# Kernel optimization log

Hardware: AMD Instinct MI355X
Metric: run time of the kernel (lower is better)

Reference implementation:

```python
import jax, jax.numpy as jnp
import numpy as np

B, N, IN_DIM, HID = 16, 2048, 128, 128
EPS = 1e-5


def _layer(x, W, b, g, beta):
    # x: (B, N, d_in) -> (B, N, HID)
    h = jnp.einsum('bnd,dh->bnh', x, W) + b
    mu = jnp.mean(h, axis=-1, keepdims=True)
    var = jnp.mean((h - mu) ** 2, axis=-1, keepdims=True)
    h = (h - mu) * jax.lax.rsqrt(var + EPS) * g + beta
    return jax.nn.relu(h)


def setup_inputs() -> dict:
    key = jax.random.key(0)
    ks = jax.random.split(key, 8)
    x = jax.random.normal(ks[0], (B, N, IN_DIM), dtype=jnp.float32)
    adj = jax.random.uniform(ks[1], (B, N, N), dtype=jnp.float32)
    inp = {'x': x, 'adj': adj}
    dims = [IN_DIM, HID, HID]
    for i in range(3):
        d_in = dims[i]
        scale = 1.0 / np.sqrt(d_in)
        inp[f'W{i}'] = jax.random.uniform(ks[2 + i], (d_in, HID), dtype=jnp.float32, minval=-scale, maxval=scale)
        inp[f'b{i}'] = jax.random.uniform(ks[5 + i], (HID,), dtype=jnp.float32, minval=-scale, maxval=scale)
        inp[f'g{i}'] = jnp.ones((HID,), dtype=jnp.float32)
        inp[f'be{i}'] = jnp.zeros((HID,), dtype=jnp.float32)
    return inp


def reference(x, adj, W0, b0, g0, be0, W1, b1, g1, be1, W2, b2, g2, be2):
    params = [(W0, b0, g0, be0), (W1, b1, g1, be1), (W2, b2, g2, be2)]
    h = x
    for (W, b, g, beta) in params:
        h_agg = jnp.einsum('bnm,bmd->bnd', adj, h)  # dense adjacency aggregation
        h = _layer(h_agg, W, b, g, beta)
    return h
```

## Files before the change

kernel.cpp:

```cpp
#include <hip/hip_runtime.h>
#include <hip/hip_bf16.h>

typedef __bf16 bf16;
typedef __bf16 bf16x4 __attribute__((ext_vector_type(4)));
typedef __bf16 bf16x8 __attribute__((ext_vector_type(8)));
typedef float  f32x2  __attribute__((ext_vector_type(2)));
typedef float  f32x4  __attribute__((ext_vector_type(4)));

static constexpr int NB  = 16;
static constexpr int NN  = 2048;
static constexpr int HID = 128;

__device__ __forceinline__ void gload_lds16(const bf16* g, bf16* l) {
    __builtin_amdgcn_global_load_lds(
        (const __attribute__((address_space(1))) unsigned int*)g,
        (__attribute__((address_space(3))) unsigned int*)l, 16, 0, 0);
}

__global__ __launch_bounds__(256) void prep_wt(const float* __restrict__ W0,
                                               const float* __restrict__ W1,
                                               const float* __restrict__ W2,
                                               bf16* __restrict__ WT) {
    int l = blockIdx.x;
    const float* W = (l == 0) ? W0 : (l == 1) ? W1 : W2;
    bf16* out = WT + l * 128 * 128;
    int tid = threadIdx.x;
#pragma unroll
    for (int i = 0; i < 64; ++i) {
        int idx = i * 256 + tid;
        int k = idx >> 7, n = idx & 127;
        out[n * 128 + k] = (bf16)W[idx];
    }
}

template<typename TA>
__global__ __launch_bounds__(256) void small_gemm(const TA* __restrict__ A,
                                                  const bf16* __restrict__ WT,
                                                  bf16* __restrict__ tmpT) {
    __shared__ bf16 smem[2 * 128 * 72];
    bf16* As = smem;
    bf16* Bs = smem + 128 * 72;

    const int tid  = threadIdx.x;
    const int wave = tid >> 6, lane = tid & 63;
    const int c0 = lane & 15, q = lane >> 4;
    const int blk = blockIdx.x;
    const int row_g0 = blk * 128;

    f32x4 acc[2][8] = {};

    for (int kk = 0; kk < 2; ++kk) {
        const int k0 = kk * 64;
        if constexpr (sizeof(TA) == 4) {
#pragma unroll
            for (int i = 0; i < 8; ++i) {
                int flat = i * 1024 + tid * 4;
                int row = flat >> 6, col = flat & 63;
                f32x4 v = *(const f32x4*)(A + (size_t)(row_g0 + row) * 128 + k0 + col);
                bf16x4 o = { (bf16)v.x, (bf16)v.y, (bf16)v.z, (bf16)v.w };
                *(bf16x4*)(As + row * 72 + col) = o;
            }
        } else {
#pragma unroll
            for (int i = 0; i < 4; ++i) {
                int flat = i * 2048 + tid * 8;
                int row = flat >> 6, col = flat & 63;
                bf16x8 v = *(const bf16x8*)((const bf16*)A + (size_t)(row_g0 + row) * 128 + k0 + col);
                *(bf16x8*)(As + row * 72 + col) = v;
            }
        }
#pragma unroll
        for (int i = 0; i < 4; ++i) {
            int flat = i * 2048 + tid * 8;
            int row = flat >> 6, col = flat & 63;
            bf16x8 v = *(const bf16x8*)(WT + (size_t)row * 128 + k0 + col);
            *(bf16x8*)(Bs + row * 72 + col) = v;
        }
        __syncthreads();
#pragma unroll
        for (int ks = 0; ks < 2; ++ks) {
            bf16x8 af[2];
#pragma unroll
            for (int mt = 0; mt < 2; ++mt)
                af[mt] = *(const bf16x8*)(As + (wave * 32 + mt * 16 + c0) * 72 + ks * 32 + q * 8);
#pragma unroll
            for (int nt = 0; nt < 8; ++nt) {
                bf16x8 bfr = *(const bf16x8*)(Bs + (nt * 16 + c0) * 72 + ks * 32 + q * 8);
#pragma unroll
                for (int mt = 0; mt < 2; ++mt)
                    acc[mt][nt] = __builtin_amdgcn_mfma_f32_16x16x32_bf16(af[mt], bfr, acc[mt][nt], 0, 0, 0);
            }
        }
        __syncthreads();
    }

    bf16* Cs = smem;
#pragma unroll
    for (int mt = 0; mt < 2; ++mt) {
        int mbase = wave * 32 + mt * 16 + q * 4;
#pragma unroll
        for (int nt = 0; nt < 8; ++nt) {
            int n = nt * 16 + c0;
#pragma unroll
            for (int r = 0; r < 4; ++r)
                Cs[n * 136 + mbase + r] = (bf16)acc[mt][nt][r];
        }
    }
    __syncthreads();
    const int b    = blk >> 4;
    const int row0 = (blk & 15) * 128;
    bf16* outp = tmpT + (size_t)b * 128 * 2048;
#pragma unroll
    for (int i = 0; i < 8; ++i) {
        int flat = i * 2048 + tid * 8;
        int n = flat >> 7, m = flat & 127;
        bf16x8 v = *(const bf16x8*)(Cs + n * 136 + m);
        *(bf16x8*)(outp + (size_t)n * 2048 + row0 + m) = v;
    }
}

template<int AMODE>
__global__ __launch_bounds__(256, 2) void big_gemm(const float* __restrict__ Af,
                                                   bf16* __restrict__ adjB,
                                                   const bf16* __restrict__ Bt,
                                                   float* __restrict__ part) {
    __shared__ bf16 As[128 * 64];
    __shared__ bf16 Bs[128 * 64];

    const int tid  = threadIdx.x;
    const int wave = tid >> 6, lane = tid & 63;
    const int c0 = lane & 15, q = lane >> 4;
    const int m0  = blockIdx.x * 128;
    const int ksp = blockIdx.y;
    const int b   = blockIdx.z;
    const size_t abase = (size_t)b * NN * NN;
    const bf16* Btb = Bt + (size_t)b * HID * NN;
    const int mrow = (wave >> 1) * 64, ncol = (wave & 1) * 64;

    f32x4 acc[4][4] = {};

    int prow[4], pcb[4];
#pragma unroll
    for (int j = 0; j < 4; ++j) {
        int p = j * 256 + wave * 64 + lane;
        prow[j] = p >> 3;
        pcb[j]  = (p & 7) ^ (prow[j] & 7);
    }
    const int ldsbase = wave * 64 * 8;

    for (int kk = 0; kk < 16; ++kk) {
        const int k0 = ksp * 1024 + kk * 64;
        if constexpr (AMODE == 1) {
#pragma unroll
            for (int j = 0; j < 4; ++j) {
                int g = j * 256 + tid;
                int grow = g >> 3, gcb = g & 7;
                const float* src = Af + abase + (size_t)(m0 + grow) * NN + k0 + gcb * 8;
                f32x4 a  = *(const f32x4*)src;
                f32x4 b2 = *(const f32x4*)(src + 4);
                bf16x8 o = {(bf16)a.x, (bf16)a.y, (bf16)a.z, (bf16)a.w,
                            (bf16)b2.x, (bf16)b2.y, (bf16)b2.z, (bf16)b2.w};
                *(bf16x8*)(As + (grow * 8 + (gcb ^ (grow & 7))) * 8) = o;
                *(bf16x8*)(adjB + abase + (size_t)(m0 + grow) * NN + k0 + gcb * 8) = o;
            }
        } else {
#pragma unroll
            for (int j = 0; j < 4; ++j)
                gload_lds16(adjB + abase + (size_t)(m0 + prow[j]) * NN + k0 + pcb[j] * 8,
                            As + j * 2048 + ldsbase);
        }
#pragma unroll
        for (int j = 0; j < 4; ++j)
            gload_lds16(Btb + (size_t)prow[j] * NN + k0 + pcb[j] * 8,
                        Bs + j * 2048 + ldsbase);
        __syncthreads();
#pragma unroll
        for (int ks = 0; ks < 2; ++ks) {
            bf16x8 af[4], bfr[4];
#pragma unroll
            for (int mt = 0; mt < 4; ++mt) {
                int row = mrow + mt * 16 + c0;
                int cb  = (ks * 4 + q) ^ (row & 7);
                af[mt] = *(const bf16x8*)(As + row * 64 + cb * 8);
            }
#pragma unroll
            for (int nt = 0; nt < 4; ++nt) {
                int row = ncol + nt * 16 + c0;
                int cb  = (ks * 4 + q) ^ (row & 7);
                bfr[nt] = *(const bf16x8*)(Bs + row * 64 + cb * 8);
            }
#pragma unroll
            for (int mt = 0; mt < 4; ++mt)
#pragma unroll
                for (int nt = 0; nt < 4; ++nt)
                    acc[mt][nt] = __builtin_amdgcn_mfma_f32_16x16x32_bf16(af[mt], bfr[nt], acc[mt][nt], 0, 0, 0);
        }
        __syncthreads();
    }

    float* pb = part + ((size_t)(ksp * NB + b) * NN + m0) * HID;
#pragma unroll
    for (int mt = 0; mt < 4; ++mt)
#pragma unroll
        for (int r = 0; r < 4; ++r) {
            int m = mrow + mt * 16 + q * 4 + r;
#pragma unroll
            for (int nt = 0; nt < 4; ++nt) {
                int n = ncol + nt * 16 + c0;
                pb[(size_t)m * HID + n] = acc[mt][nt][r];
            }
        }
}

template<bool OUTF32>
__global__ __launch_bounds__(256) void reduce_ln(const float* __restrict__ part,
                                                 const float* __restrict__ bias,
                                                 const float* __restrict__ gamma,
                                                 const float* __restrict__ betap,
                                                 bf16* __restrict__ outB,
                                                 float* __restrict__ outF) {
    const int tid = threadIdx.x, wave = tid >> 6, lane = tid & 63;
    const size_t row = (size_t)blockIdx.x * 4 + wave;
    const size_t off = row * HID + lane * 2;
    f32x2 p0 = *(const f32x2*)(part + off);
    f32x2 p1 = *(const f32x2*)(part + (size_t)NB * NN * HID + off);
    f32x2 bv = *(const f32x2*)(bias + lane * 2);
    float x0 = p0.x + p1.x + bv.x;
    float x1 = p0.y + p1.y + bv.y;
    float s1 = x0 + x1, s2 = x0 * x0 + x1 * x1;
#pragma unroll
    for (int o = 1; o < 64; o <<= 1) { s1 += __shfl_xor(s1, o); s2 += __shfl_xor(s2, o); }
    float mu  = s1 * (1.f / 128.f);
    float var = s2 * (1.f / 128.f) - mu * mu;
    float rs  = rsqrtf(var + 1e-5f);
    f32x2 gv = *(const f32x2*)(gamma + lane * 2);
    f32x2 be = *(const f32x2*)(betap + lane * 2);
    float o0 = fmaxf((x0 - mu) * rs * gv.x + be.x, 0.f);
    float o1 = fmaxf((x1 - mu) * rs * gv.y + be.y, 0.f);
    if constexpr (OUTF32) {
        f32x2 o = {o0, o1};
        *(f32x2*)(outF + off) = o;
    } else {
        bf16* p = outB + off;
        p[0] = (bf16)o0; p[1] = (bf16)o1;
    }
}

extern "C" void kernel_launch(void* const* d_in, const int* in_sizes, int n_in,
                              void* d_out, int out_size, void* d_ws, size_t ws_size,
                              hipStream_t stream) {
    const float* x   = (const float*)d_in[0];
    const float* adj = (const float*)d_in[1];
    const float* W[3]  = {(const float*)d_in[2],  (const float*)d_in[6],  (const float*)d_in[10]};
    const float* bb[3] = {(const float*)d_in[3],  (const float*)d_in[7],  (const float*)d_in[11]};
    const float* gg[3] = {(const float*)d_in[4],  (const float*)d_in[8],  (const float*)d_in[12]};
    const float* be[3] = {(const float*)d_in[5],  (const float*)d_in[9],  (const float*)d_in[13]};

    char* ws = (char*)d_ws;
    size_t off = 0;
    auto alloc = [&](size_t bytes) { char* p = ws + off; off = (off + bytes + 255) & ~(size_t)255; return p; };
    bf16*  WT   = (bf16*) alloc((size_t)3 * 128 * 128 * 2);
    bf16*  tmpT = (bf16*) alloc((size_t)NB * HID * NN * 2);
    bf16*  hB   = (bf16*) alloc((size_t)NB * NN * HID * 2);
    bf16*  adjB = (bf16*) alloc((size_t)NB * NN * NN * 2);
    float* part = (float*)alloc((size_t)2 * NB * NN * HID * 4);

    float* outF = (float*)d_out;

    prep_wt<<<3, 256, 0, stream>>>(W[0], W[1], W[2], WT);

    dim3 bg(16, 2, 16);
    small_gemm<float><<<256, 256, 0, stream>>>(x, WT, tmpT);
    big_gemm<1><<<bg, 256, 0, stream>>>(adj, adjB, tmpT, part);
    reduce_ln<false><<<8192, 256, 0, stream>>>(part, bb[0], gg[0], be[0], hB, nullptr);
    small_gemm<bf16><<<256, 256, 0, stream>>>(hB, WT + 128 * 128, tmpT);
    big_gemm<2><<<bg, 256, 0, stream>>>(adj, adjB, tmpT, part);
    reduce_ln<false><<<8192, 256, 0, stream>>>(part, bb[1], gg[1], be[1], hB, nullptr);
    small_gemm<bf16><<<256, 256, 0, stream>>>(hB, WT + 2 * 128 * 128, tmpT);
    big_gemm<2><<<bg, 256, 0, stream>>>(adj, adjB, tmpT, part);
    reduce_ln<true><<<8192, 256, 0, stream>>>(part, bb[2], gg[2], be[2], nullptr, outF);
}
```

Baseline: 583.9 us.

## Reorder to aggregate-then-project, fuse projection with LayerNorm, drop split-K

The per-layer order changes from (x·W then adj·) to (adj·h then ·W), which matches the reference order. The small projection GEMM is fused with bias, LayerNorm and ReLU into one kernel that writes the transposed bf16 activations for the next layer. The big adjacency GEMM drops the 2-way split-K and fp32 partial buffers in favour of 64-row tiles over the full K, writing bf16 output directly. This removes the separate reduce kernel and its fp32 partial traffic. The cost is a longer per-block K loop, smaller M tiles with less B reuse, and extra rounding from storing the aggregate in bf16.

New measurement: 556.6 us. 1.05x faster.

```diff
diff --git a/kernel.cpp b/kernel.cpp
--- a/kernel.cpp
+++ b/kernel.cpp
@@ -33,89 +33,26 @@
     }
 }
 
-template<typename TA>
-__global__ __launch_bounds__(256) void small_gemm(const TA* __restrict__ A,
-                                                  const bf16* __restrict__ WT,
-                                                  bf16* __restrict__ tmpT) {
-    __shared__ bf16 smem[2 * 128 * 72];
-    bf16* As = smem;
-    bf16* Bs = smem + 128 * 72;
-
-    const int tid  = threadIdx.x;
-    const int wave = tid >> 6, lane = tid & 63;
-    const int c0 = lane & 15, q = lane >> 4;
+__global__ __launch_bounds__(256) void prep_xt(const float* __restrict__ x,
+                                               bf16* __restrict__ xT) {
+    __shared__ bf16 T[128 * 136];
     const int blk = blockIdx.x;
-    const int row_g0 = blk * 128;
-
-    f32x4 acc[2][8] = {};
-
-    for (int kk = 0; kk < 2; ++kk) {
-        const int k0 = kk * 64;
-        if constexpr (sizeof(TA) == 4) {
-#pragma unroll
-            for (int i = 0; i < 8; ++i) {
-                int flat = i * 1024 + tid * 4;
-                int row = flat >> 6, col = flat & 63;
-                f32x4 v = *(const f32x4*)(A + (size_t)(row_g0 + row) * 128 + k0 + col);
-                bf16x4 o = { (bf16)v.x, (bf16)v.y, (bf16)v.z, (bf16)v.w };
-                *(bf16x4*)(As + row * 72 + col) = o;
-            }
-        } else {
-#pragma unroll
-            for (int i = 0; i < 4; ++i) {
-                int flat = i * 2048 + tid * 8;
-                int row = flat >> 6, col = flat & 63;
-                bf16x8 v = *(const bf16x8*)((const bf16*)A + (size_t)(row_g0 + row) * 128 + k0 + col);
-                *(bf16x8*)(As + row * 72 + col) = v;
-            }
-        }
-#pragma unroll
-        for (int i = 0; i < 4; ++i) {
-            int flat = i * 2048 + tid * 8;
-            int row = flat >> 6, col = flat & 63;
-            bf16x8 v = *(const bf16x8*)(WT + (size_t)row * 128 + k0 + col);
-            *(bf16x8*)(Bs + row * 72 + col) = v;
-        }
-        __syncthreads();
-#pragma unroll
-        for (int ks = 0; ks < 2; ++ks) {
-            bf16x8 af[2];
-#pragma unroll
-            for (int mt = 0; mt < 2; ++mt)
-                af[mt] = *(const bf16x8*)(As + (wave * 32 + mt * 16 + c0) * 72 + ks * 32 + q * 8);
-#pragma unroll
-            for (int nt = 0; nt < 8; ++nt) {
-                bf16x8 bfr = *(const bf16x8*)(Bs + (nt * 16 + c0) * 72 + ks * 32 + q * 8);
-#pragma unroll
-                for (int mt = 0; mt < 2; ++mt)
-                    acc[mt][nt] = __builtin_amdgcn_mfma_f32_16x16x32_bf16(af[mt], bfr, acc[mt][nt], 0, 0, 0);
-            }
-        }
-        __syncthreads();
-    }
-
-    bf16* Cs = smem;
-#pragma unroll
-    for (int mt = 0; mt < 2; ++mt) {
-        int mbase = wave * 32 + mt * 16 + q * 4;
-#pragma unroll
-        for (int nt = 0; nt < 8; ++nt) {
-            int n = nt * 16 + c0;
-#pragma unroll
-            for (int r = 0; r < 4; ++r)
-                Cs[n * 136 + mbase + r] = (bf16)acc[mt][nt][r];
-        }
+    const int b = blk >> 4, node0 = (blk & 15) * 128;
+    const int tid = threadIdx.x;
+    const float* xb = x + ((size_t)b * NN + node0) * HID;
+#pragma unroll
+    for (int i = 0; i < 64; ++i) {
+        int idx = i * 256 + tid;
+        int node = idx >> 7, hid = idx & 127;
+        T[hid * 136 + node] = (bf16)xb[(size_t)node * HID + hid];
     }
     __syncthreads();
-    const int b    = blk >> 4;
-    const int row0 = (blk & 15) * 128;
-    bf16* outp = tmpT + (size_t)b * 128 * 2048;
+    bf16* ob = xT + (size_t)b * HID * NN + node0;
 #pragma unroll
     for (int i = 0; i < 8; ++i) {
         int flat = i * 2048 + tid * 8;
-        int n = flat >> 7, m = flat & 127;
-        bf16x8 v = *(const bf16x8*)(Cs + n * 136 + m);
-        *(bf16x8*)(outp + (size_t)n * 2048 + row0 + m) = v;
+        int hid = flat >> 7, node = flat & 127;
+        *(bf16x8*)(ob + (size_t)hid * NN + node) = *(const bf16x8*)(T + hid * 136 + node);
     }
 }
 
@@ -123,21 +60,20 @@
 __global__ __launch_bounds__(256, 2) void big_gemm(const float* __restrict__ Af,
                                                    bf16* __restrict__ adjB,
                                                    const bf16* __restrict__ Bt,
-                                                   float* __restrict__ part) {
-    __shared__ bf16 As[128 * 64];
+                                                   bf16* __restrict__ g) {
+    __shared__ bf16 As[64 * 64];
     __shared__ bf16 Bs[128 * 64];
 
     const int tid  = threadIdx.x;
     const int wave = tid >> 6, lane = tid & 63;
     const int c0 = lane & 15, q = lane >> 4;
-    const int m0  = blockIdx.x * 128;
-    const int ksp = blockIdx.y;
-    const int b   = blockIdx.z;
+    const int m0 = blockIdx.x * 64;
+    const int b  = blockIdx.z;
     const size_t abase = (size_t)b * NN * NN;
     const bf16* Btb = Bt + (size_t)b * HID * NN;
-    const int mrow = (wave >> 1) * 64, ncol = (wave & 1) * 64;
-
-    f32x4 acc[4][4] = {};
+    const int wm = wave >> 1, wn = wave & 1;
+
+    f32x4 acc[2][4] = {};
 
     int prow[4], pcb[4];
 #pragma unroll
@@ -146,15 +82,15 @@
         prow[j] = p >> 3;
         pcb[j]  = (p & 7) ^ (prow[j] & 7);
     }
-    const int ldsbase = wave * 64 * 8;
-
-    for (int kk = 0; kk < 16; ++kk) {
-        const int k0 = ksp * 1024 + kk * 64;
+    const int ldsbase = wave * 512;
+
+    for (int kk = 0; kk < 32; ++kk) {
+        const int k0 = kk * 64;
         if constexpr (AMODE == 1) {
 #pragma unroll
-            for (int j = 0; j < 4; ++j) {
-                int g = j * 256 + tid;
-                int grow = g >> 3, gcb = g & 7;
+            for (int j = 0; j < 2; ++j) {
+                int gi = j * 256 + tid;
+                int grow = gi >> 3, gcb = gi & 7;
                 const float* src = Af + abase + (size_t)(m0 + grow) * NN + k0 + gcb * 8;
                 f32x4 a  = *(const f32x4*)src;
                 f32x4 b2 = *(const f32x4*)(src + 4);
@@ -165,7 +101,7 @@
             }
         } else {
 #pragma unroll
-            for (int j = 0; j < 4; ++j)
+            for (int j = 0; j < 2; ++j)
                 gload_lds16(adjB + abase + (size_t)(m0 + prow[j]) * NN + k0 + pcb[j] * 8,
                             As + j * 2048 + ldsbase);
         }
@@ -176,21 +112,21 @@
         __syncthreads();
 #pragma unroll
         for (int ks = 0; ks < 2; ++ks) {
-            bf16x8 af[4], bfr[4];
-#pragma unroll
-            for (int mt = 0; mt < 4; ++mt) {
-                int row = mrow + mt * 16 + c0;
+            bf16x8 af[2], bfr[4];
+#pragma unroll
+            for (int mt = 0; mt < 2; ++mt) {
+                int row = wm * 32 + mt * 16 + c0;
                 int cb  = (ks * 4 + q) ^ (row & 7);
                 af[mt] = *(const bf16x8*)(As + row * 64 + cb * 8);
             }
 #pragma unroll
             for (int nt = 0; nt < 4; ++nt) {
-                int row = ncol + nt * 16 + c0;
+                int row = wn * 64 + nt * 16 + c0;
                 int cb  = (ks * 4 + q) ^ (row & 7);
                 bfr[nt] = *(const bf16x8*)(Bs + row * 64 + cb * 8);
             }
 #pragma unroll
-            for (int mt = 0; mt < 4; ++mt)
+            for (int mt = 0; mt < 2; ++mt)
 #pragma unroll
                 for (int nt = 0; nt < 4; ++nt)
                     acc[mt][nt] = __builtin_amdgcn_mfma_f32_16x16x32_bf16(af[mt], bfr[nt], acc[mt][nt], 0, 0, 0);
@@ -198,51 +134,126 @@
         __syncthreads();
     }
 
-    float* pb = part + ((size_t)(ksp * NB + b) * NN + m0) * HID;
-#pragma unroll
-    for (int mt = 0; mt < 4; ++mt)
+    bf16* gb = g + ((size_t)b * NN + m0) * HID;
+#pragma unroll
+    for (int mt = 0; mt < 2; ++mt)
 #pragma unroll
         for (int r = 0; r < 4; ++r) {
-            int m = mrow + mt * 16 + q * 4 + r;
+            int m = wm * 32 + mt * 16 + q * 4 + r;
 #pragma unroll
             for (int nt = 0; nt < 4; ++nt) {
-                int n = ncol + nt * 16 + c0;
-                pb[(size_t)m * HID + n] = acc[mt][nt][r];
-            }
-        }
-}
-
-template<bool OUTF32>
-__global__ __launch_bounds__(256) void reduce_ln(const float* __restrict__ part,
-                                                 const float* __restrict__ bias,
-                                                 const float* __restrict__ gamma,
-                                                 const float* __restrict__ betap,
-                                                 bf16* __restrict__ outB,
-                                                 float* __restrict__ outF) {
-    const int tid = threadIdx.x, wave = tid >> 6, lane = tid & 63;
-    const size_t row = (size_t)blockIdx.x * 4 + wave;
-    const size_t off = row * HID + lane * 2;
-    f32x2 p0 = *(const f32x2*)(part + off);
-    f32x2 p1 = *(const f32x2*)(part + (size_t)NB * NN * HID + off);
-    f32x2 bv = *(const f32x2*)(bias + lane * 2);
-    float x0 = p0.x + p1.x + bv.x;
-    float x1 = p0.y + p1.y + bv.y;
-    float s1 = x0 + x1, s2 = x0 * x0 + x1 * x1;
-#pragma unroll
-    for (int o = 1; o < 64; o <<= 1) { s1 += __shfl_xor(s1, o); s2 += __shfl_xor(s2, o); }
-    float mu  = s1 * (1.f / 128.f);
-    float var = s2 * (1.f / 128.f) - mu * mu;
-    float rs  = rsqrtf(var + 1e-5f);
-    f32x2 gv = *(const f32x2*)(gamma + lane * 2);
-    f32x2 be = *(const f32x2*)(betap + lane * 2);
-    float o0 = fmaxf((x0 - mu) * rs * gv.x + be.x, 0.f);
-    float o1 = fmaxf((x1 - mu) * rs * gv.y + be.y, 0.f);
-    if constexpr (OUTF32) {
-        f32x2 o = {o0, o1};
-        *(f32x2*)(outF + off) = o;
-    } else {
-        bf16* p = outB + off;
-        p[0] = (bf16)o0; p[1] = (bf16)o1;
+                int n = wn * 64 + nt * 16 + c0;
+                gb[(size_t)m * HID + n] = (bf16)acc[mt][nt][r];
+            }
+        }
+}
+
+template<bool FINAL>
+__global__ __launch_bounds__(256) void small_ln(const bf16* __restrict__ gin,
+                                                const bf16* __restrict__ WT,
+                                                const float* __restrict__ bias,
+                                                const float* __restrict__ gamma,
+                                                const float* __restrict__ betap,
+                                                bf16* __restrict__ hT,
+                                                float* __restrict__ outF) {
+    __shared__ bf16 smem[2 * 128 * 72];
+    bf16* As = smem;
+    bf16* Bs = smem + 128 * 72;
+
+    const int tid  = threadIdx.x;
+    const int wave = tid >> 6, lane = tid & 63;
+    const int c0 = lane & 15, q = lane >> 4;
+    const int blk = blockIdx.x;
+    const int row_g0 = blk * 128;
+
+    f32x4 acc[2][8] = {};
+
+    for (int kk = 0; kk < 2; ++kk) {
+        const int k0 = kk * 64;
+#pragma unroll
+        for (int i = 0; i < 4; ++i) {
+            int flat = i * 2048 + tid * 8;
+            int row = flat >> 6, col = flat & 63;
+            bf16x8 v = *(const bf16x8*)(gin + (size_t)(row_g0 + row) * HID + k0 + col);
+            *(bf16x8*)(As + row * 72 + col) = v;
+        }
+#pragma unroll
+        for (int i = 0; i < 4; ++i) {
+            int flat = i * 2048 + tid * 8;
+            int row = flat >> 6, col = flat & 63;
+            bf16x8 v = *(const bf16x8*)(WT + (size_t)row * 128 + k0 + col);
+            *(bf16x8*)(Bs + row * 72 + col) = v;
+        }
+        __syncthreads();
+#pragma unroll
+        for (int ks = 0; ks < 2; ++ks) {
+            bf16x8 af[2];
+#pragma unroll
+            for (int mt = 0; mt < 2; ++mt)
+                af[mt] = *(const bf16x8*)(As + (wave * 32 + mt * 16 + c0) * 72 + ks * 32 + q * 8);
+#pragma unroll
+            for (int nt = 0; nt < 8; ++nt) {
+                bf16x8 bfr = *(const bf16x8*)(Bs + (nt * 16 + c0) * 72 + ks * 32 + q * 8);
+#pragma unroll
+                for (int mt = 0; mt < 2; ++mt)
+                    acc[mt][nt] = __builtin_amdgcn_mfma_f32_16x16x32_bf16(af[mt], bfr, acc[mt][nt], 0, 0, 0);
+            }
+        }
+        __syncthreads();
+    }
+
+    float bv[8], gv[8], bev[8];
+#pragma unroll
+    for (int nt = 0; nt < 8; ++nt) {
+        int n = nt * 16 + c0;
+        bv[nt] = bias[n]; gv[nt] = gamma[n]; bev[nt] = betap[n];
+    }
+    bf16* Cs = smem;
+#pragma unroll
+    for (int mt = 0; mt < 2; ++mt) {
+#pragma unroll
+        for (int r = 0; r < 4; ++r) {
+            float v[8], s1 = 0.f, s2 = 0.f;
+#pragma unroll
+            for (int nt = 0; nt < 8; ++nt) {
+                float xv = acc[mt][nt][r] + bv[nt];
+                v[nt] = xv; s1 += xv; s2 += xv * xv;
+            }
+#pragma unroll
+            for (int off = 1; off < 16; off <<= 1) {
+                s1 += __shfl_xor(s1, off);
+                s2 += __shfl_xor(s2, off);
+            }
+            float mu  = s1 * (1.f / 128.f);
+            float var = s2 * (1.f / 128.f) - mu * mu;
+            float rs  = rsqrtf(var + 1e-5f);
+            int m = wave * 32 + mt * 16 + q * 4 + r;
+            if constexpr (FINAL) {
+                size_t rowoff = ((size_t)row_g0 + m) * HID;
+#pragma unroll
+                for (int nt = 0; nt < 8; ++nt) {
+                    float o = fmaxf((v[nt] - mu) * rs * gv[nt] + bev[nt], 0.f);
+                    outF[rowoff + nt * 16 + c0] = o;
+                }
+            } else {
+#pragma unroll
+                for (int nt = 0; nt < 8; ++nt) {
+                    float o = fmaxf((v[nt] - mu) * rs * gv[nt] + bev[nt], 0.f);
+                    Cs[(nt * 16 + c0) * 136 + m] = (bf16)o;
+                }
+            }
+        }
+    }
+    if constexpr (!FINAL) {
+        __syncthreads();
+        const int b = blk >> 4, row0 = (blk & 15) * 128;
+        bf16* outp = hT + (size_t)b * HID * NN;
+#pragma unroll
+        for (int i = 0; i < 8; ++i) {
+            int flat = i * 2048 + tid * 8;
+            int n = flat >> 7, mm = flat & 127;
+            *(bf16x8*)(outp + (size_t)n * NN + row0 + mm) = *(const bf16x8*)(Cs + n * 136 + mm);
+        }
     }
 }
 
@@ -259,24 +270,22 @@
     char* ws = (char*)d_ws;
     size_t off = 0;
     auto alloc = [&](size_t bytes) { char* p = ws + off; off = (off + bytes + 255) & ~(size_t)255; return p; };
-    bf16*  WT   = (bf16*) alloc((size_t)3 * 128 * 128 * 2);
-    bf16*  tmpT = (bf16*) alloc((size_t)NB * HID * NN * 2);
-    bf16*  hB   = (bf16*) alloc((size_t)NB * NN * HID * 2);
-    bf16*  adjB = (bf16*) alloc((size_t)NB * NN * NN * 2);
-    float* part = (float*)alloc((size_t)2 * NB * NN * HID * 4);
+    bf16* WT   = (bf16*)alloc((size_t)3 * 128 * 128 * 2);
+    bf16* xT   = (bf16*)alloc((size_t)NB * HID * NN * 2);
+    bf16* hT   = (bf16*)alloc((size_t)NB * HID * NN * 2);
+    bf16* gbuf = (bf16*)alloc((size_t)NB * NN * HID * 2);
+    bf16* adjB = (bf16*)alloc((size_t)NB * NN * NN * 2);
 
     float* outF = (float*)d_out;
 
     prep_wt<<<3, 256, 0, stream>>>(W[0], W[1], W[2], WT);
-
-    dim3 bg(16, 2, 16);
-    small_gemm<float><<<256, 256, 0, stream>>>(x, WT, tmpT);
-    big_gemm<1><<<bg, 256, 0, stream>>>(adj, adjB, tmpT, part);
-    reduce_ln<false><<<8192, 256, 0, stream>>>(part, bb[0], gg[0], be[0], hB, nullptr);
-    small_gemm<bf16><<<256, 256, 0, stream>>>(hB, WT + 128 * 128, tmpT);
-    big_gemm<2><<<bg, 256, 0, stream>>>(adj, adjB, tmpT, part);
-    reduce_ln<false><<<8192, 256, 0, stream>>>(part, bb[1], gg[1], be[1], hB, nullptr);
-    small_gemm<bf16><<<256, 256, 0, stream>>>(hB, WT + 2 * 128 * 128, tmpT);
-    big_gemm<2><<<bg, 256, 0, stream>>>(adj, adjB, tmpT, part);
-    reduce_ln<true><<<8192, 256, 0, stream>>>(part, bb[2], gg[2], be[2], nullptr, outF);
-}
+    prep_xt<<<256, 256, 0, stream>>>(x, xT);
+
+    dim3 bg(32, 1, 16);
+    big_gemm<1><<<bg, 256, 0, stream>>>(adj, adjB, xT, gbuf);
+    small_ln<false><<<256, 256, 0, stream>>>(gbuf, WT, bb[0], gg[0], be[0], hT, nullptr);
+    big_gemm<2><<<bg, 256, 0, stream>>>(adj, adjB, hT, gbuf);
+    small_ln<false><<<256, 256, 0, stream>>>(gbuf, WT + 128 * 128, bb[1], gg[1], be[1], hT, nullptr);
+    big_gemm<2><<<bg, 256, 0, stream>>>(adj, adjB, hT, gbuf);
+    small_ln<true><<<256, 256, 0, stream>>>(gbuf, WT + 2 * 128 * 128, bb[2], gg[2], be[2], nullptr, outF);
+}
```
